# Optimization experiments

Measured on AMD Instinct MI355X. Metric: run time of the kernel, lower is better.

Reference implementation:

```python
import jax, jax.numpy as jnp
import numpy as np

N, D, U, E, B = 8192, 1024, 512, 8, 8


def setup_inputs() -> dict:
    key = jax.random.key(0)
    ks = jax.random.split(key, 8)
    x = jax.random.normal(ks[0], (N, D), dtype=jnp.float32)
    # stacked per-expert parameters (Dense + KolmogorovLayer)
    W1 = jax.random.normal(ks[1], (E, D, U), dtype=jnp.float32) * 0.02
    b1 = jnp.zeros((E, U), dtype=jnp.float32)
    proj = jax.random.normal(ks[2], (E, U, U), dtype=jnp.float32) * 0.02
    ctrl = jax.random.normal(ks[3], (E, B, U), dtype=jnp.float32) * 0.1
    scaling = jnp.ones((E, U), dtype=jnp.float32)
    # gating Dense
    Wg = jax.random.normal(ks[4], (D, E), dtype=jnp.float32) * 0.02
    bg = jnp.zeros((E,), dtype=jnp.float32)
    return {"x": x, "W1": W1, "b1": b1, "proj": proj, "ctrl": ctrl,
            "scaling": scaling, "Wg": Wg, "bg": bg}


def reference(x, W1, b1, proj, ctrl, scaling, Wg, bg):
    num_bases = ctrl.shape[1]
    # expert Dense + swish: [E, N, U]
    h = jax.nn.swish(jnp.einsum('nd,edu->enu', x, W1) + b1[:, None, :])
    # KolmogorovLayer: projection -> sigmoid -> gaussian-RBF B-spline basis
    z = jnp.einsum('enu,euv->env', h, proj)
    xn = jax.nn.sigmoid(z)                                   # [E, N, U] in (0,1)
    knots = jnp.linspace(0.0, 1.0, num_bases)                # [B]
    dist = (xn[..., None] - knots) ** 2                      # [E, N, U, B]
    basis = jnp.exp(-dist / (2.0 * (1.0 / num_bases) ** 2))
    basis = basis / (jnp.sum(basis, axis=-1, keepdims=True) + 1e-6)
    # contract bases with control points per unit, then scale: [E, N, U]
    expert_out = jnp.einsum('enub,ebu->enu', basis, ctrl) * scaling[:, None, :]
    # gating (inference path): hard one-hot argmax of logits
    logits = x @ Wg + bg                                     # [N, E]
    gate = jax.nn.one_hot(jnp.argmax(logits, axis=-1), logits.shape[-1],
                          dtype=x.dtype)                     # [N, E]
    # weighted sum over experts -> [N, U]
    return jnp.einsum('enu,ne->nu', expert_out, gate)
```

## Files before the change

### kernel.cpp

```cpp
#include <hip/hip_runtime.h>
#include <hip/hip_bf16.h>
#include <stdint.h>

#define NTOK 8192
#define DDIM 1024
#define UDIM 512
#define NEXP 8
#define MT_MAX 136

typedef __attribute__((ext_vector_type(8))) short bf16x8;
typedef __attribute__((ext_vector_type(4))) float f32x4;


__device__ __forceinline__ unsigned short f2bf(float f) {
  unsigned int u = __float_as_uint(f);
  u += 0x7FFFu + ((u >> 16) & 1u);
  return (unsigned short)(u >> 16);
}

__device__ __forceinline__ void gload16(const void* g, void* lds) {
  __builtin_amdgcn_global_load_lds(
      (__attribute__((address_space(1))) void*)(uintptr_t)g,
      (__attribute__((address_space(3))) void*)(uint32_t)(uintptr_t)lds,
      16, 0, 0);
}


__global__ __launch_bounds__(256) void k_prep_pack(
    const float* __restrict__ x, const float* __restrict__ Wg,
    const float* __restrict__ bg, const float* __restrict__ W1,
    const float* __restrict__ proj, unsigned short* __restrict__ xbf,
    int* __restrict__ eidx, unsigned short* __restrict__ W1p,
    unsigned short* __restrict__ projp) {
  __shared__ __align__(16) char smem[8 * 1040 * 4];
  const int t = threadIdx.x;

  if (blockIdx.x < 2048) {
    float (*WgT)[1040] = (float(*)[1040])smem;
#pragma unroll
    for (int r = 0; r < 32; ++r)
      WgT[t & 7][r * 32 + (t >> 3)] = Wg[r * 256 + t];
    __syncthreads();

    const int lane = t & 63;
    const int n = (blockIdx.x << 2) + (t >> 6);
    const float* xr = x + (size_t)n * DDIM;
    unsigned short* xo = xbf + (size_t)n * DDIM;
    float acc[8] = {0.f, 0.f, 0.f, 0.f, 0.f, 0.f, 0.f, 0.f};
#pragma unroll
    for (int c = 0; c < 4; ++c) {
      const int d = c * 256 + lane * 4;
      const float4 xv = *(const float4*)(xr + d);
      ushort4 o;
      o.x = f2bf(xv.x); o.y = f2bf(xv.y); o.z = f2bf(xv.z); o.w = f2bf(xv.w);
      *(ushort4*)(xo + d) = o;
#pragma unroll
      for (int e = 0; e < 8; ++e) {
        const float4 wv = *(const float4*)(&WgT[e][d]);
        acc[e] = fmaf(xv.x, wv.x, acc[e]);
        acc[e] = fmaf(xv.y, wv.y, acc[e]);
        acc[e] = fmaf(xv.z, wv.z, acc[e]);
        acc[e] = fmaf(xv.w, wv.w, acc[e]);
      }
    }
#pragma unroll
    for (int e = 0; e < 8; ++e) {
#pragma unroll
      for (int o = 32; o > 0; o >>= 1) acc[e] += __shfl_xor(acc[e], o, 64);
    }
    if (lane == 0) {
      int best = 0;
      float bv = acc[0] + bg[0];
#pragma unroll
      for (int e2 = 1; e2 < 8; ++e2) {
        const float v = acc[e2] + bg[e2];
        if (v > bv) { bv = v; best = e2; }
      }
      eidx[n] = best;
    }
  } else {
    float (*tile)[65] = (float(*)[65])smem;
    const int id = blockIdx.x - 2048;
    const int c0 = (id & 7) << 6;
    const int r0 = ((id >> 3) & 15) << 6;
    const int z = id >> 7;
    const int R = (z < 8) ? DDIM : UDIM;
    if (r0 >= R) return;
    const float* src = (z < 8) ? (W1 + (size_t)z * DDIM * UDIM)
                               : (proj + (size_t)(z - 8) * UDIM * UDIM);
    unsigned short* dst = (z < 8) ? (W1p + (size_t)z * DDIM * UDIM)
                                  : (projp + (size_t)(z - 8) * UDIM * UDIM);
#pragma unroll
    for (int i = 0; i < 4; ++i) {
      const int ri = (t >> 4) + i * 16;
      const int ci = (t & 15) * 4;
      const float4 v = *(const float4*)(src + (size_t)(r0 + ri) * UDIM + c0 + ci);
      tile[ri][ci] = v.x; tile[ri][ci + 1] = v.y; tile[ri][ci + 2] = v.z; tile[ri][ci + 3] = v.w;
    }
    __syncthreads();
    const int cc = t >> 2, ch = t & 3;
#pragma unroll
    for (int j = 0; j < 2; ++j) {
      const int kt = (r0 >> 5) + j;
      union { bf16x8 v; unsigned short u[8]; } pk;
#pragma unroll
      for (int q = 0; q < 8; ++q) pk.u[q] = f2bf(tile[j * 32 + ch * 8 + q][cc]);
      *(bf16x8*)(dst + ((size_t)kt * UDIM + c0 + cc) * 32 + ch * 8) = pk.v;
    }
  }
}


__global__ __launch_bounds__(1024) void k_sort(const int* __restrict__ eidx,
                                               int* __restrict__ perm_p,
                                               int* __restrict__ tile_expert,
                                               int* __restrict__ tile_rowlim) {
  __shared__ int wavetot[8][16];
  __shared__ int tot[8];
  __shared__ int tbase[9];
  const int t = threadIdx.x;
  const int lane = t & 63, wid = t >> 6;

  int my[8], c[8] = {0, 0, 0, 0, 0, 0, 0, 0};
#pragma unroll
  for (int i = 0; i < 8; ++i) {
    my[i] = eidx[t * 8 + i];
#pragma unroll
    for (int b = 0; b < 8; ++b) c[b] += (my[i] == b);
  }

  int inc[8];
#pragma unroll
  for (int b = 0; b < 8; ++b) {
    int v = c[b];
#pragma unroll
    for (int o = 1; o < 64; o <<= 1) {
      const int u = __shfl_up(v, o, 64);
      if (lane >= o) v += u;
    }
    inc[b] = v;
  }
  if (lane == 63) {
#pragma unroll
    for (int b = 0; b < 8; ++b) wavetot[b][wid] = inc[b];
  }
  __syncthreads();

  if (t < 8) {
    int run = 0;
#pragma unroll
    for (int w2 = 0; w2 < 16; ++w2) {
      const int u = wavetot[t][w2];
      wavetot[t][w2] = run;
      run += u;
    }
    tot[t] = run;
  }
  __syncthreads();
  if (t == 0) {
    int run = 0;
    for (int e = 0; e < 8; ++e) { tbase[e] = run; run += (tot[e] + 63) >> 6; }
    tbase[8] = run;
  }
  __syncthreads();

  int base[8];
#pragma unroll
  for (int b = 0; b < 8; ++b)
    base[b] = (tbase[b] << 6) + wavetot[b][wid] + inc[b] - c[b];
#pragma unroll
  for (int b = 0; b < 8; ++b) {
    int p = base[b];
#pragma unroll
    for (int i = 0; i < 8; ++i)
      if (my[i] == b) perm_p[p++] = t * 8 + i;
  }

  if (t < MT_MAX) {
    int e = -1, rl = 0;
#pragma unroll
    for (int q = 0; q < 8; ++q) {
      if (t >= tbase[q] && t < tbase[q + 1]) {
        e = q;
        const int r = tot[q] - (t - tbase[q]) * 64;
        rl = r < 64 ? r : 64;
      }
    }
    tile_expert[t] = e;
    tile_rowlim[t] = rl;
  }
}


__global__ __launch_bounds__(256) void k_gemm1(
    const unsigned short* __restrict__ xbf, const unsigned short* __restrict__ W1p,
    const float* __restrict__ b1, const int* __restrict__ perm_p,
    const int* __restrict__ tile_expert, const int* __restrict__ tile_rowlim,
    unsigned short* __restrict__ Hp) {
  __shared__ __align__(16) short Ab[3][64 * 32];
  __shared__ __align__(16) short Bb[3][64 * 32];
  __shared__ int rows_s[64];

  const int orig = blockIdx.x;
  const int wg = (orig & 7) * MT_MAX + (orig >> 3);
  const int Mt = wg >> 3, Nt = wg & 7;
  const int e = tile_expert[Mt];
  if (e < 0) return;
  const int rowlim = tile_rowlim[Mt];

  const int t = threadIdx.x;
  const int w = t >> 6, wr = w >> 1, wc = w & 1;
  const int lane = t & 63, ln15 = lane & 15, g = lane >> 4;

  if (t < 64) rows_s[t] = perm_p[Mt * 64 + (t < rowlim ? t : 0)];
  __syncthreads();

  const int srow = t >> 2;
  const int sh = (t & 3) ^ ((srow >> 1) & 3);
  const unsigned short* arow = xbf + (size_t)rows_s[srow] * DDIM + sh * 8;
  const unsigned short* Bpan = W1p + ((size_t)e * 32 * UDIM + Nt * 64) * 32;

  auto stage = [&](int kt, int buf) {
    gload16(arow + kt * 32, (char*)Ab[buf] + (t & ~63) * 16);
    gload16(Bpan + (size_t)kt * UDIM * 32 + srow * 32 + sh * 8,
            (char*)Bb[buf] + (t & ~63) * 16);
  };

  f32x4 acc[2][2];
  const f32x4 z4 = {0.f, 0.f, 0.f, 0.f};
  acc[0][0] = z4; acc[0][1] = z4; acc[1][0] = z4; acc[1][1] = z4;

  stage(0, 0);
  stage(1, 1);
  const int NK = 32;
  int cur = 0;
  for (int kt = 0; kt < NK; ++kt) {
    __builtin_amdgcn_sched_barrier(0);
    if (kt + 1 < NK) asm volatile("s_waitcnt vmcnt(2)" ::: "memory");
    else             asm volatile("s_waitcnt vmcnt(0)" ::: "memory");
    __builtin_amdgcn_s_barrier();
    __builtin_amdgcn_sched_barrier(0);

    bf16x8 af[2], bf_[2];
#pragma unroll
    for (int mt = 0; mt < 2; ++mt) {
      const int r = wr * 32 + mt * 16 + ln15;
      af[mt] = *(const bf16x8*)((const char*)Ab[cur] + r * 64 + (g ^ ((r >> 1) & 3)) * 16);
    }
#pragma unroll
    for (int nt = 0; nt < 2; ++nt) {
      const int c2 = wc * 32 + nt * 16 + ln15;
      bf_[nt] = *(const bf16x8*)((const char*)Bb[cur] + c2 * 64 + (g ^ ((c2 >> 1) & 3)) * 16);
    }
#pragma unroll
    for (int mt = 0; mt < 2; ++mt)
#pragma unroll
      for (int nt = 0; nt < 2; ++nt)
        acc[mt][nt] = __builtin_amdgcn_mfma_f32_16x16x32_bf16(af[mt], bf_[nt], acc[mt][nt], 0, 0, 0);

    if (kt + 2 < NK) stage(kt + 2, (cur + 2) % 3);
    cur = (cur + 1) % 3;
  }

  float bv[2];
#pragma unroll
  for (int nt = 0; nt < 2; ++nt)
    bv[nt] = b1[e * UDIM + Nt * 64 + wc * 32 + nt * 16 + ln15];
#pragma unroll
  for (int mt = 0; mt < 2; ++mt) {
#pragma unroll
    for (int nt = 0; nt < 2; ++nt) {
      const int colg = Nt * 64 + wc * 32 + nt * 16 + ln15;
      unsigned short* hp = Hp + ((size_t)(Mt * 16 + (colg >> 5)) * 64) * 32 + (colg & 31);
#pragma unroll
      for (int r = 0; r < 4; ++r) {
        const int row = wr * 32 + mt * 16 + g * 4 + r;
        const float a = acc[mt][nt][r] + bv[nt];
        hp[(size_t)row * 32] = f2bf(a * __builtin_amdgcn_rcpf(1.f + __expf(-a)));
      }
    }
  }
}


__global__ __launch_bounds__(256) void k_gemm2(
    const unsigned short* __restrict__ Hp, const unsigned short* __restrict__ projp,
    const float* __restrict__ ctrl, const float* __restrict__ scaling,
    const int* __restrict__ perm_p, const int* __restrict__ tile_expert,
    const int* __restrict__ tile_rowlim, float* __restrict__ out) {
  __shared__ __align__(16) short Ab[3][64 * 32];
  __shared__ __align__(16) short Bb[3][64 * 32];
  __shared__ int tok_s[64];

  const int orig = blockIdx.x;
  const int wg = (orig & 7) * MT_MAX + (orig >> 3);
  const int Mt = wg >> 3, Nt = wg & 7;
  const int e = tile_expert[Mt];
  if (e < 0) return;
  const int rowlim = tile_rowlim[Mt];

  const int t = threadIdx.x;
  const int w = t >> 6, wr = w >> 1, wc = w & 1;
  const int lane = t & 63, ln15 = lane & 15, g = lane >> 4;

  if (t < 64) tok_s[t] = perm_p[Mt * 64 + (t < rowlim ? t : 0)];
  __syncthreads();

  const int srow = t >> 2;
  const int sh = (t & 3) ^ ((srow >> 1) & 3);
  const unsigned short* Apan = Hp + ((size_t)Mt * 16 * 64) * 32;
  const unsigned short* Bpan = projp + ((size_t)e * 16 * UDIM + Nt * 64) * 32;

  auto stage = [&](int kt, int buf) {
    gload16(Apan + (size_t)kt * 64 * 32 + srow * 32 + sh * 8,
            (char*)Ab[buf] + (t & ~63) * 16);
    gload16(Bpan + (size_t)kt * UDIM * 32 + srow * 32 + sh * 8,
            (char*)Bb[buf] + (t & ~63) * 16);
  };

  f32x4 acc[2][2];
  const f32x4 z4 = {0.f, 0.f, 0.f, 0.f};
  acc[0][0] = z4; acc[0][1] = z4; acc[1][0] = z4; acc[1][1] = z4;

  stage(0, 0);
  stage(1, 1);
  const int NK = 16;
  int cur = 0;
  for (int kt = 0; kt < NK; ++kt) {
    __builtin_amdgcn_sched_barrier(0);
    if (kt + 1 < NK) asm volatile("s_waitcnt vmcnt(2)" ::: "memory");
    else             asm volatile("s_waitcnt vmcnt(0)" ::: "memory");
    __builtin_amdgcn_s_barrier();
    __builtin_amdgcn_sched_barrier(0);

    bf16x8 af[2], bf_[2];
#pragma unroll
    for (int mt = 0; mt < 2; ++mt) {
      const int r = wr * 32 + mt * 16 + ln15;
      af[mt] = *(const bf16x8*)((const char*)Ab[cur] + r * 64 + (g ^ ((r >> 1) & 3)) * 16);
    }
#pragma unroll
    for (int nt = 0; nt < 2; ++nt) {
      const int c2 = wc * 32 + nt * 16 + ln15;
      bf_[nt] = *(const bf16x8*)((const char*)Bb[cur] + c2 * 64 + (g ^ ((c2 >> 1) & 3)) * 16);
    }
#pragma unroll
    for (int mt = 0; mt < 2; ++mt)
#pragma unroll
      for (int nt = 0; nt < 2; ++nt)
        acc[mt][nt] = __builtin_amdgcn_mfma_f32_16x16x32_bf16(af[mt], bf_[nt], acc[mt][nt], 0, 0, 0);

    if (kt + 2 < NK) stage(kt + 2, (cur + 2) % 3);
    cur = (cur + 1) % 3;
  }

  const float M = 0.27086949f;
  float cv[2][8], sc[2];
#pragma unroll
  for (int nt = 0; nt < 2; ++nt) {
    const int colg = Nt * 64 + wc * 32 + nt * 16 + ln15;
    sc[nt] = scaling[e * UDIM + colg];
#pragma unroll
    for (int b = 0; b < 8; ++b) cv[nt][b] = ctrl[((size_t)e * 8 + b) * UDIM + colg];
  }
#pragma unroll
  for (int mt = 0; mt < 2; ++mt) {
#pragma unroll
    for (int r = 0; r < 4; ++r) {
      const int row = wr * 32 + mt * 16 + g * 4 + r;
      if (row < rowlim) {
        const int tok = tok_s[row];
#pragma unroll
        for (int nt = 0; nt < 2; ++nt) {
          const int colg = Nt * 64 + wc * 32 + nt * 16 + ln15;
          const float z = acc[mt][nt][r];
          const float xn = __builtin_amdgcn_rcpf(1.f + __expf(-z));
          float q = __expf(-32.f * xn * xn);
          float rr = __expf(xn * (64.f / 7.f) - (32.f / 49.f));
          float s = 0.f, dc = 0.f;
#pragma unroll
          for (int b = 0; b < 8; ++b) {
            s += q;
            dc = fmaf(q, cv[nt][b], dc);
            q *= rr;
            rr *= M;
          }
          out[(size_t)tok * UDIM + colg] = dc * __builtin_amdgcn_rcpf(s + 1e-6f) * sc[nt];
        }
      }
    }
  }
}


extern "C" void kernel_launch(void* const* d_in, const int* in_sizes, int n_in,
                              void* d_out, int out_size, void* d_ws, size_t ws_size,
                              hipStream_t stream) {
  const float* x       = (const float*)d_in[0];
  const float* W1      = (const float*)d_in[1];
  const float* b1      = (const float*)d_in[2];
  const float* proj    = (const float*)d_in[3];
  const float* ctrl    = (const float*)d_in[4];
  const float* scaling = (const float*)d_in[5];
  const float* Wg      = (const float*)d_in[6];
  const float* bg      = (const float*)d_in[7];
  float* out = (float*)d_out;
  char* ws = (char*)d_ws;

  int* eidx        = (int*)(ws + 0);
  int* perm_p      = (int*)(ws + 32768);
  int* tile_expert = (int*)(ws + 69632 + 64);
  int* tile_rowlim = (int*)(ws + 69632 + 640);
  unsigned short* W1p   = (unsigned short*)(ws + 131072);
  unsigned short* projp = (unsigned short*)(ws + 131072 + 8388608);
  unsigned short* Hp    = (unsigned short*)(ws + 131072 + 8388608 + 4194304);
  unsigned short* xbf   = (unsigned short*)(ws + 131072 + 8388608 + 4194304 + 9175040);

  k_prep_pack<<<4096, 256, 0, stream>>>(x, Wg, bg, W1, proj, xbf, eidx, W1p, projp);
  k_sort<<<1, 1024, 0, stream>>>(eidx, perm_p, tile_expert, tile_rowlim);
  k_gemm1<<<MT_MAX * 8, 256, 0, stream>>>(xbf, W1p, b1, perm_p,
                                          tile_expert, tile_rowlim, Hp);
  k_gemm2<<<MT_MAX * 8, 256, 0, stream>>>(Hp, projp, ctrl, scaling, perm_p,
                                          tile_expert, tile_rowlim, out);
}
```

Baseline: 67.13 us.

## Halve GEMM N-tile to 32, double-buffer with syncthreads, batch 4 tokens per wave in prep

Both grouped GEMMs change from 64x64 to 64x32 output tiles, with each wave owning a 16-row strip. The grid doubles and launch bounds request 8 blocks per CU. The three-stage pipeline with manual vmcnt waits becomes a simpler two-buffer loop with __syncthreads, meant to raise occupancy and parallelism. The prep kernel now processes four tokens per wave, which cuts the number of gating blocks and reduces per-block Wg transposes into LDS. The cost is that the A tile is reloaded twice as often and the latency hiding from the deeper pipeline is lost.

```diff
diff --git a/kernel.cpp b/kernel.cpp
--- a/kernel.cpp
+++ b/kernel.cpp
@@ -35,7 +35,7 @@
   __shared__ __align__(16) char smem[8 * 1040 * 4];
   const int t = threadIdx.x;
 
-  if (blockIdx.x < 2048) {
+  if (blockIdx.x < 512) {
     float (*WgT)[1040] = (float(*)[1040])smem;
 #pragma unroll
     for (int r = 0; r < 32; ++r)
@@ -43,44 +43,62 @@
     __syncthreads();
 
     const int lane = t & 63;
-    const int n = (blockIdx.x << 2) + (t >> 6);
-    const float* xr = x + (size_t)n * DDIM;
-    unsigned short* xo = xbf + (size_t)n * DDIM;
-    float acc[8] = {0.f, 0.f, 0.f, 0.f, 0.f, 0.f, 0.f, 0.f};
+    const int wid = t >> 6;
+    const int n0 = (blockIdx.x << 4) + (wid << 2);
+    float acc[4][8];
+#pragma unroll
+    for (int i = 0; i < 4; ++i)
+#pragma unroll
+      for (int e = 0; e < 8; ++e) acc[i][e] = 0.f;
+
 #pragma unroll
     for (int c = 0; c < 4; ++c) {
       const int d = c * 256 + lane * 4;
-      const float4 xv = *(const float4*)(xr + d);
-      ushort4 o;
-      o.x = f2bf(xv.x); o.y = f2bf(xv.y); o.z = f2bf(xv.z); o.w = f2bf(xv.w);
-      *(ushort4*)(xo + d) = o;
+      float4 xv[4];
+#pragma unroll
+      for (int i = 0; i < 4; ++i)
+        xv[i] = *(const float4*)(x + (size_t)(n0 + i) * DDIM + d);
+#pragma unroll
+      for (int i = 0; i < 4; ++i) {
+        ushort4 o;
+        o.x = f2bf(xv[i].x); o.y = f2bf(xv[i].y); o.z = f2bf(xv[i].z); o.w = f2bf(xv[i].w);
+        *(ushort4*)(xbf + (size_t)(n0 + i) * DDIM + d) = o;
+      }
 #pragma unroll
       for (int e = 0; e < 8; ++e) {
         const float4 wv = *(const float4*)(&WgT[e][d]);
-        acc[e] = fmaf(xv.x, wv.x, acc[e]);
-        acc[e] = fmaf(xv.y, wv.y, acc[e]);
-        acc[e] = fmaf(xv.z, wv.z, acc[e]);
-        acc[e] = fmaf(xv.w, wv.w, acc[e]);
-      }
-    }
-#pragma unroll
-    for (int e = 0; e < 8; ++e) {
-#pragma unroll
-      for (int o = 32; o > 0; o >>= 1) acc[e] += __shfl_xor(acc[e], o, 64);
-    }
+#pragma unroll
+        for (int i = 0; i < 4; ++i) {
+          acc[i][e] = fmaf(xv[i].x, wv.x, acc[i][e]);
+          acc[i][e] = fmaf(xv[i].y, wv.y, acc[i][e]);
+          acc[i][e] = fmaf(xv[i].z, wv.z, acc[i][e]);
+          acc[i][e] = fmaf(xv[i].w, wv.w, acc[i][e]);
+        }
+      }
+    }
+#pragma unroll
+    for (int i = 0; i < 4; ++i)
+#pragma unroll
+      for (int e = 0; e < 8; ++e) {
+#pragma unroll
+        for (int o = 32; o > 0; o >>= 1) acc[i][e] += __shfl_xor(acc[i][e], o, 64);
+      }
     if (lane == 0) {
-      int best = 0;
-      float bv = acc[0] + bg[0];
-#pragma unroll
-      for (int e2 = 1; e2 < 8; ++e2) {
-        const float v = acc[e2] + bg[e2];
-        if (v > bv) { bv = v; best = e2; }
-      }
-      eidx[n] = best;
+#pragma unroll
+      for (int i = 0; i < 4; ++i) {
+        int best = 0;
+        float bv = acc[i][0] + bg[0];
+#pragma unroll
+        for (int e2 = 1; e2 < 8; ++e2) {
+          const float v = acc[i][e2] + bg[e2];
+          if (v > bv) { bv = v; best = e2; }
+        }
+        eidx[n0 + i] = best;
+      }
     }
   } else {
     float (*tile)[65] = (float(*)[65])smem;
-    const int id = blockIdx.x - 2048;
+    const int id = blockIdx.x - 512;
     const int c0 = (id & 7) << 6;
     const int r0 = ((id >> 3) & 15) << 6;
     const int z = id >> 7;
@@ -192,201 +210,178 @@
 }
 
 
-__global__ __launch_bounds__(256) void k_gemm1(
+__global__ __launch_bounds__(256, 8) void k_gemm1(
     const unsigned short* __restrict__ xbf, const unsigned short* __restrict__ W1p,
     const float* __restrict__ b1, const int* __restrict__ perm_p,
     const int* __restrict__ tile_expert, const int* __restrict__ tile_rowlim,
     unsigned short* __restrict__ Hp) {
-  __shared__ __align__(16) short Ab[3][64 * 32];
-  __shared__ __align__(16) short Bb[3][64 * 32];
+  __shared__ __align__(16) short Ab[2][64 * 32];
+  __shared__ __align__(16) short Bb[2][32 * 32];
   __shared__ int rows_s[64];
 
   const int orig = blockIdx.x;
-  const int wg = (orig & 7) * MT_MAX + (orig >> 3);
-  const int Mt = wg >> 3, Nt = wg & 7;
+  const int wg = (orig & 7) * 272 + (orig >> 3);
+  const int Mt = wg >> 4, Nt = wg & 15;
   const int e = tile_expert[Mt];
   if (e < 0) return;
   const int rowlim = tile_rowlim[Mt];
 
   const int t = threadIdx.x;
-  const int w = t >> 6, wr = w >> 1, wc = w & 1;
+  const int w = t >> 6;
   const int lane = t & 63, ln15 = lane & 15, g = lane >> 4;
 
   if (t < 64) rows_s[t] = perm_p[Mt * 64 + (t < rowlim ? t : 0)];
   __syncthreads();
 
-  const int srow = t >> 2;
-  const int sh = (t & 3) ^ ((srow >> 1) & 3);
-  const unsigned short* arow = xbf + (size_t)rows_s[srow] * DDIM + sh * 8;
-  const unsigned short* Bpan = W1p + ((size_t)e * 32 * UDIM + Nt * 64) * 32;
+  const int arow = t >> 2;
+  const int ah = (t & 3) ^ ((arow >> 1) & 3);
+  const unsigned short* asrc = xbf + (size_t)rows_s[arow] * DDIM + ah * 8;
+  const int bcol = t >> 2;
+  const int bh = (t & 3) ^ ((bcol >> 1) & 3);
+  const unsigned short* Bpan = W1p + ((size_t)e * 32 * UDIM + Nt * 32) * 32;
 
   auto stage = [&](int kt, int buf) {
-    gload16(arow + kt * 32, (char*)Ab[buf] + (t & ~63) * 16);
-    gload16(Bpan + (size_t)kt * UDIM * 32 + srow * 32 + sh * 8,
-            (char*)Bb[buf] + (t & ~63) * 16);
+    gload16(asrc + kt * 32, (char*)Ab[buf] + (t & ~63) * 16);
+    if (t < 128)
+      gload16(Bpan + (size_t)kt * UDIM * 32 + bcol * 32 + bh * 8,
+              (char*)Bb[buf] + (t & ~63) * 16);
   };
 
-  f32x4 acc[2][2];
+  f32x4 acc[2];
   const f32x4 z4 = {0.f, 0.f, 0.f, 0.f};
-  acc[0][0] = z4; acc[0][1] = z4; acc[1][0] = z4; acc[1][1] = z4;
+  acc[0] = z4; acc[1] = z4;
 
   stage(0, 0);
-  stage(1, 1);
-  const int NK = 32;
+  __syncthreads();
   int cur = 0;
-  for (int kt = 0; kt < NK; ++kt) {
-    __builtin_amdgcn_sched_barrier(0);
-    if (kt + 1 < NK) asm volatile("s_waitcnt vmcnt(2)" ::: "memory");
-    else             asm volatile("s_waitcnt vmcnt(0)" ::: "memory");
-    __builtin_amdgcn_s_barrier();
-    __builtin_amdgcn_sched_barrier(0);
-
-    bf16x8 af[2], bf_[2];
-#pragma unroll
-    for (int mt = 0; mt < 2; ++mt) {
-      const int r = wr * 32 + mt * 16 + ln15;
-      af[mt] = *(const bf16x8*)((const char*)Ab[cur] + r * 64 + (g ^ ((r >> 1) & 3)) * 16);
-    }
+  const int r = w * 16 + ln15;
+  const int aslot = g ^ ((r >> 1) & 3);
+  for (int kt = 0; kt < 32; ++kt) {
+    const int nb = cur ^ 1;
+    if (kt < 31) stage(kt + 1, nb);
+    bf16x8 af, bf_[2];
+    af = *(const bf16x8*)((const char*)Ab[cur] + r * 64 + aslot * 16);
 #pragma unroll
     for (int nt = 0; nt < 2; ++nt) {
-      const int c2 = wc * 32 + nt * 16 + ln15;
+      const int c2 = nt * 16 + ln15;
       bf_[nt] = *(const bf16x8*)((const char*)Bb[cur] + c2 * 64 + (g ^ ((c2 >> 1) & 3)) * 16);
     }
 #pragma unroll
-    for (int mt = 0; mt < 2; ++mt)
-#pragma unroll
-      for (int nt = 0; nt < 2; ++nt)
-        acc[mt][nt] = __builtin_amdgcn_mfma_f32_16x16x32_bf16(af[mt], bf_[nt], acc[mt][nt], 0, 0, 0);
-
-    if (kt + 2 < NK) stage(kt + 2, (cur + 2) % 3);
-    cur = (cur + 1) % 3;
-  }
-
-  float bv[2];
-#pragma unroll
-  for (int nt = 0; nt < 2; ++nt)
-    bv[nt] = b1[e * UDIM + Nt * 64 + wc * 32 + nt * 16 + ln15];
-#pragma unroll
-  for (int mt = 0; mt < 2; ++mt) {
-#pragma unroll
-    for (int nt = 0; nt < 2; ++nt) {
-      const int colg = Nt * 64 + wc * 32 + nt * 16 + ln15;
-      unsigned short* hp = Hp + ((size_t)(Mt * 16 + (colg >> 5)) * 64) * 32 + (colg & 31);
-#pragma unroll
-      for (int r = 0; r < 4; ++r) {
-        const int row = wr * 32 + mt * 16 + g * 4 + r;
-        const float a = acc[mt][nt][r] + bv[nt];
-        hp[(size_t)row * 32] = f2bf(a * __builtin_amdgcn_rcpf(1.f + __expf(-a)));
-      }
-    }
-  }
-}
-
-
-__global__ __launch_bounds__(256) void k_gemm2(
+    for (int nt = 0; nt < 2; ++nt)
+      acc[nt] = __builtin_amdgcn_mfma_f32_16x16x32_bf16(af, bf_[nt], acc[nt], 0, 0, 0);
+    __syncthreads();
+    cur = nb;
+  }
+
+  unsigned short* hp = Hp + ((size_t)(Mt * 16 + Nt) * 64) * 32;
+#pragma unroll
+  for (int nt = 0; nt < 2; ++nt) {
+    const int cin = nt * 16 + ln15;
+    const float bv = b1[e * UDIM + Nt * 32 + cin];
+#pragma unroll
+    for (int rr = 0; rr < 4; ++rr) {
+      const int row = w * 16 + g * 4 + rr;
+      const float a = acc[nt][rr] + bv;
+      hp[row * 32 + cin] = f2bf(a * __builtin_amdgcn_rcpf(1.f + __expf(-a)));
+    }
+  }
+}
+
+
+__global__ __launch_bounds__(256, 8) void k_gemm2(
     const unsigned short* __restrict__ Hp, const unsigned short* __restrict__ projp,
     const float* __restrict__ ctrl, const float* __restrict__ scaling,
     const int* __restrict__ perm_p, const int* __restrict__ tile_expert,
     const int* __restrict__ tile_rowlim, float* __restrict__ out) {
-  __shared__ __align__(16) short Ab[3][64 * 32];
-  __shared__ __align__(16) short Bb[3][64 * 32];
+  __shared__ __align__(16) short Ab[2][64 * 32];
+  __shared__ __align__(16) short Bb[2][32 * 32];
   __shared__ int tok_s[64];
 
   const int orig = blockIdx.x;
-  const int wg = (orig & 7) * MT_MAX + (orig >> 3);
-  const int Mt = wg >> 3, Nt = wg & 7;
+  const int wg = (orig & 7) * 272 + (orig >> 3);
+  const int Mt = wg >> 4, Nt = wg & 15;
   const int e = tile_expert[Mt];
   if (e < 0) return;
   const int rowlim = tile_rowlim[Mt];
 
   const int t = threadIdx.x;
-  const int w = t >> 6, wr = w >> 1, wc = w & 1;
+  const int w = t >> 6;
   const int lane = t & 63, ln15 = lane & 15, g = lane >> 4;
 
   if (t < 64) tok_s[t] = perm_p[Mt * 64 + (t < rowlim ? t : 0)];
   __syncthreads();
 
-  const int srow = t >> 2;
-  const int sh = (t & 3) ^ ((srow >> 1) & 3);
+  const int arow = t >> 2;
+  const int ah = (t & 3) ^ ((arow >> 1) & 3);
+  const int bcol = t >> 2;
+  const int bh = (t & 3) ^ ((bcol >> 1) & 3);
   const unsigned short* Apan = Hp + ((size_t)Mt * 16 * 64) * 32;
-  const unsigned short* Bpan = projp + ((size_t)e * 16 * UDIM + Nt * 64) * 32;
+  const unsigned short* Bpan = projp + ((size_t)e * 16 * UDIM + Nt * 32) * 32;
 
   auto stage = [&](int kt, int buf) {
-    gload16(Apan + (size_t)kt * 64 * 32 + srow * 32 + sh * 8,
+    gload16(Apan + (size_t)kt * 64 * 32 + arow * 32 + ah * 8,
             (char*)Ab[buf] + (t & ~63) * 16);
-    gload16(Bpan + (size_t)kt * UDIM * 32 + srow * 32 + sh * 8,
-            (char*)Bb[buf] + (t & ~63) * 16);
+    if (t < 128)
+      gload16(Bpan + (size_t)kt * UDIM * 32 + bcol * 32 + bh * 8,
+              (char*)Bb[buf] + (t & ~63) * 16);
   };
 
-  f32x4 acc[2][2];
+  f32x4 acc[2];
   const f32x4 z4 = {0.f, 0.f, 0.f, 0.f};
-  acc[0][0] = z4; acc[0][1] = z4; acc[1][0] = z4; acc[1][1] = z4;
+  acc[0] = z4; acc[1] = z4;
 
   stage(0, 0);
-  stage(1, 1);
-  const int NK = 16;
+  __syncthreads();
   int cur = 0;
-  for (int kt = 0; kt < NK; ++kt) {
-    __builtin_amdgcn_sched_barrier(0);
-    if (kt + 1 < NK) asm volatile("s_waitcnt vmcnt(2)" ::: "memory");
-    else             asm volatile("s_waitcnt vmcnt(0)" ::: "memory");
-    __builtin_amdgcn_s_barrier();
-    __builtin_amdgcn_sched_barrier(0);
-
-    bf16x8 af[2], bf_[2];
-#pragma unroll
-    for (int mt = 0; mt < 2; ++mt) {
-      const int r = wr * 32 + mt * 16 + ln15;
-      af[mt] = *(const bf16x8*)((const char*)Ab[cur] + r * 64 + (g ^ ((r >> 1) & 3)) * 16);
-    }
+  const int r = w * 16 + ln15;
+  const int aslot = g ^ ((r >> 1) & 3);
+  for (int kt = 0; kt < 16; ++kt) {
+    const int nb = cur ^ 1;
+    if (kt < 15) stage(kt + 1, nb);
+    bf16x8 af, bf_[2];
+    af = *(const bf16x8*)((const char*)Ab[cur] + r * 64 + aslot * 16);
 #pragma unroll
     for (int nt = 0; nt < 2; ++nt) {
-      const int c2 = wc * 32 + nt * 16 + ln15;
+      const int c2 = nt * 16 + ln15;
       bf_[nt] = *(const bf16x8*)((const char*)Bb[cur] + c2 * 64 + (g ^ ((c2 >> 1) & 3)) * 16);
     }
 #pragma unroll
-    for (int mt = 0; mt < 2; ++mt)
-#pragma unroll
-      for (int nt = 0; nt < 2; ++nt)
-        acc[mt][nt] = __builtin_amdgcn_mfma_f32_16x16x32_bf16(af[mt], bf_[nt], acc[mt][nt], 0, 0, 0);
-
-    if (kt + 2 < NK) stage(kt + 2, (cur + 2) % 3);
-    cur = (cur + 1) % 3;
+    for (int nt = 0; nt < 2; ++nt)
+      acc[nt] = __builtin_amdgcn_mfma_f32_16x16x32_bf16(af, bf_[nt], acc[nt], 0, 0, 0);
+    __syncthreads();
+    cur = nb;
   }
 
   const float M = 0.27086949f;
   float cv[2][8], sc[2];
 #pragma unroll
   for (int nt = 0; nt < 2; ++nt) {
-    const int colg = Nt * 64 + wc * 32 + nt * 16 + ln15;
+    const int colg = Nt * 32 + nt * 16 + ln15;
     sc[nt] = scaling[e * UDIM + colg];
 #pragma unroll
     for (int b = 0; b < 8; ++b) cv[nt][b] = ctrl[((size_t)e * 8 + b) * UDIM + colg];
   }
 #pragma unroll
-  for (int mt = 0; mt < 2; ++mt) {
-#pragma unroll
-    for (int r = 0; r < 4; ++r) {
-      const int row = wr * 32 + mt * 16 + g * 4 + r;
-      if (row < rowlim) {
-        const int tok = tok_s[row];
-#pragma unroll
-        for (int nt = 0; nt < 2; ++nt) {
-          const int colg = Nt * 64 + wc * 32 + nt * 16 + ln15;
-          const float z = acc[mt][nt][r];
-          const float xn = __builtin_amdgcn_rcpf(1.f + __expf(-z));
-          float q = __expf(-32.f * xn * xn);
-          float rr = __expf(xn * (64.f / 7.f) - (32.f / 49.f));
-          float s = 0.f, dc = 0.f;
-#pragma unroll
-          for (int b = 0; b < 8; ++b) {
-            s += q;
-            dc = fmaf(q, cv[nt][b], dc);
-            q *= rr;
-            rr *= M;
-          }
-          out[(size_t)tok * UDIM + colg] = dc * __builtin_amdgcn_rcpf(s + 1e-6f) * sc[nt];
+  for (int rr = 0; rr < 4; ++rr) {
+    const int row = w * 16 + g * 4 + rr;
+    if (row < rowlim) {
+      const int tok = tok_s[row];
+#pragma unroll
+      for (int nt = 0; nt < 2; ++nt) {
+        const int colg = Nt * 32 + nt * 16 + ln15;
+        const float z = acc[nt][rr];
+        const float xn = __builtin_amdgcn_rcpf(1.f + __expf(-z));
+        float q = __expf(-32.f * xn * xn);
+        float rt = __expf(xn * (64.f / 7.f) - (32.f / 49.f));
+        float s = 0.f, dc = 0.f;
+#pragma unroll
+        for (int b = 0; b < 8; ++b) {
+          s += q;
+          dc = fmaf(q, cv[nt][b], dc);
+          q *= rt;
+          rt *= M;
         }
+        out[(size_t)tok * UDIM + colg] = dc * __builtin_amdgcn_rcpf(s + 1e-6f) * sc[nt];
       }
     }
   }
@@ -416,10 +411,10 @@
   unsigned short* Hp    = (unsigned short*)(ws + 131072 + 8388608 + 4194304);
   unsigned short* xbf   = (unsigned short*)(ws + 131072 + 8388608 + 4194304 + 9175040);
 
-  k_prep_pack<<<4096, 256, 0, stream>>>(x, Wg, bg, W1, proj, xbf, eidx, W1p, projp);
+  k_prep_pack<<<2560, 256, 0, stream>>>(x, Wg, bg, W1, proj, xbf, eidx, W1p, projp);
   k_sort<<<1, 1024, 0, stream>>>(eidx, perm_p, tile_expert, tile_rowlim);
-  k_gemm1<<<MT_MAX * 8, 256, 0, stream>>>(xbf, W1p, b1, perm_p,
-                                          tile_expert, tile_rowlim, Hp);
-  k_gemm2<<<MT_MAX * 8, 256, 0, stream>>>(Hp, projp, ctrl, scaling, perm_p,
-                                          tile_expert, tile_rowlim, out);
-}
+  k_gemm1<<<MT_MAX * 16, 256, 0, stream>>>(xbf, W1p, b1, perm_p,
+                                           tile_expert, tile_rowlim, Hp);
+  k_gemm2<<<MT_MAX * 16, 256, 0, stream>>>(Hp, projp, ctrl, scaling, perm_p,
+                                           tile_expert, tile_rowlim, out);
+}
```

Measured after the change: 83.78 us. +24.8%, slower.
